# Kernel tuning notes

Hardware: AMD Instinct MI355X
Metric: run time of the kernel (lower is better)

Reference implementation:

```python
import jax, jax.numpy as jnp
import numpy as np

HEADS = 4
DIM_HEAD = 128


def setup_inputs() -> dict:
    key = jax.random.key(0)
    k1, k2, k3, k4 = jax.random.split(key, 4)
    b, dim, H, W = 4, 256, 128, 128
    hidden = HEADS * DIM_HEAD  # 512
    x = jax.random.normal(k1, (b, dim, H, W), dtype=jnp.float32)
    # 1x1 convs are pointwise matmuls over channels
    w_qkv = jax.random.normal(k2, (hidden * 3, dim), dtype=jnp.float32) * 0.02
    w_out = jax.random.normal(k3, (dim, hidden), dtype=jnp.float32) * 0.02
    b_out = jax.random.normal(k4, (dim,), dtype=jnp.float32) * 0.02
    return {"x": x, "w_qkv": w_qkv, "w_out": w_out, "b_out": b_out}


def reference(x, w_qkv, w_out, b_out):
    b, c, h, w = x.shape
    n = h * w
    # to_qkv: 1x1 conv (no bias) == channel matmul -> [b, 3*heads*dh, h, w]
    qkv = jnp.einsum('bchw,oc->bohw', x, w_qkv)
    # 'b (qkv heads d) h w -> qkv b heads d (h w)'
    qkv = qkv.reshape(b, 3, HEADS, DIM_HEAD, n)
    q, k, v = qkv[:, 0], qkv[:, 1], qkv[:, 2]  # each [b, heads, d, n]
    k = jax.nn.softmax(k, axis=-1)  # softmax over spatial positions
    context = jnp.einsum('bhdn,bhen->bhde', k, v)   # [b, heads, d, d]
    out = jnp.einsum('bhde,bhdn->bhen', context, q)  # [b, heads, d, n]
    out = out.reshape(b, HEADS * DIM_HEAD, h, w)
    # to_out: 1x1 conv with bias
    return jnp.einsum('bchw,oc->bohw', out, w_out) + b_out[None, :, None, None]
```

## Files before the change

### kernel.cpp

```cpp
#include <hip/hip_runtime.h>
#include <hip/hip_bf16.h>

#define HEADS 4
#define DH    128
#define CIN   256
#define NPIX  16384
#define NB    4
#define HID   512

typedef __attribute__((ext_vector_type(8))) short bf16x8;
typedef __attribute__((ext_vector_type(4))) float f32x4;

__device__ __forceinline__ unsigned short f2bfu(float f) {
    union { __hip_bfloat16 h; unsigned short u; } cv;
    cv.h = __float2bfloat16(f);
    return cv.u;
}

typedef const __attribute__((address_space(1))) unsigned char* gas_t;
typedef __attribute__((address_space(3))) unsigned char* las_t;
__device__ __forceinline__ void glds16(const void* g, void* s) {
    __builtin_amdgcn_global_load_lds((gas_t)g, (las_t)s, 16, 0, 0);
}


__global__ __launch_bounds__(256) void xt_convert2(const float* __restrict__ x,
                                                   unsigned short* __restrict__ xt2,
                                                   unsigned short* __restrict__ xbf2)
{
    __shared__ float tile[64][66];
    const int b = blockIdx.z, c0 = blockIdx.y * 64, n0 = blockIdx.x * 64;
    const int t = threadIdx.x, lane = t & 63, wid = t >> 6;
    const float* xb = x + ((size_t)b * CIN + c0) * NPIX + n0;
#pragma unroll
    for (int p = 0; p < 4; ++p) {
        const int c = p * 16 + (t >> 4);
        const int n = (t & 15) * 4;
        float4 v = *reinterpret_cast<const float4*>(xb + (size_t)c * NPIX + n);
        tile[c][n + 0] = v.x; tile[c][n + 1] = v.y;
        tile[c][n + 2] = v.z; tile[c][n + 3] = v.w;
    }
    __syncthreads();
#pragma unroll
    for (int rr = 0; rr < 2; ++rr) {
        const int tid  = wid * 2 + rr;
        const int n16l = tid >> 1, c32l = tid & 1;
        const int nl   = n16l * 16 + (lane & 15);
        const int cb   = c32l * 32 + (lane >> 4) * 8;
        unsigned short u8[8];
#pragma unroll
        for (int j = 0; j < 8; ++j) u8[j] = f2bfu(tile[cb + j][nl]);
        *reinterpret_cast<uint4*>(
            xt2 + (((size_t)b * 1024 + (n0 >> 4) + n16l) * 8 + (c0 >> 5) + c32l) * 512 + lane * 8)
            = *reinterpret_cast<const uint4*>(u8);
    }
#pragma unroll
    for (int rr = 0; rr < 2; ++rr) {
        const int tid  = wid * 2 + rr;
        const int c16l = tid >> 1, n32l = tid & 1;
        const int cr   = c16l * 16 + (lane & 15);
        const int nb   = n32l * 32 + (lane >> 4) * 8;
        unsigned short u8[8];
#pragma unroll
        for (int j = 0; j < 8; ++j) u8[j] = f2bfu(tile[cr][nb + j]);
        *reinterpret_cast<uint4*>(
            xbf2 + (((size_t)b * 16 + (c0 >> 4) + c16l) * 512 + (n0 >> 5) + n32l) * 512 + lane * 8)
            = *reinterpret_cast<const uint4*>(u8);
    }
}

__global__ __launch_bounds__(256) void wconv3(const float* __restrict__ w_qkv,
                                              const float* __restrict__ w_out,
                                              unsigned short* __restrict__ WkF,
                                              unsigned short* __restrict__ WvF,
                                              unsigned short* __restrict__ WqTF,
                                              unsigned short* __restrict__ WoF)
{
    const int t = threadIdx.x, lane = t & 63, wid = t >> 6;
    const int tile = blockIdx.x * 4 + wid;
    unsigned short u8[8];
    unsigned short* dst;
    if (tile < 256) {
        const int h = tile >> 6, d16 = (tile >> 3) & 7, c32 = tile & 7;
        const float* src = w_qkv + (size_t)(512 + h * 128 + d16 * 16 + (lane & 15)) * CIN
                         + c32 * 32 + (lane >> 4) * 8;
#pragma unroll
        for (int j = 0; j < 8; ++j) u8[j] = f2bfu(src[j]);
        dst = WkF + (size_t)tile * 512 + lane * 8;
    } else if (tile < 512) {
        const int t2 = tile - 256;
        const int h = t2 >> 6, e16 = (t2 >> 3) & 7, c32 = t2 & 7;
        const float* src = w_qkv + (size_t)(1024 + h * 128 + e16 * 16 + (lane & 15)) * CIN
                         + c32 * 32 + (lane >> 4) * 8;
#pragma unroll
        for (int j = 0; j < 8; ++j) u8[j] = f2bfu(src[j]);
        dst = WvF + (size_t)t2 * 512 + lane * 8;
    } else if (tile < 768) {
        const int t2 = tile - 512;
        const int h = t2 >> 6, c16 = (t2 >> 2) & 15, d32 = t2 & 3;
#pragma unroll
        for (int j = 0; j < 8; ++j)
            u8[j] = f2bfu(w_qkv[(size_t)(h * 128 + d32 * 32 + (lane >> 4) * 8 + j) * CIN
                                + c16 * 16 + (lane & 15)]);
        dst = WqTF + (size_t)t2 * 512 + lane * 8;
    } else {
        const int t2 = tile - 768;
        const int o16 = t2 >> 4, m32 = t2 & 15;
        const float* src = w_out + (size_t)(o16 * 16 + (lane & 15)) * HID
                         + m32 * 32 + (lane >> 4) * 8;
#pragma unroll
        for (int j = 0; j < 8; ++j) u8[j] = f2bfu(src[j]);
        dst = WoF + (size_t)t2 * 512 + lane * 8;
    }
    *reinterpret_cast<uint4*>(dst) = *reinterpret_cast<const uint4*>(u8);
}

__global__ __launch_bounds__(512, 2) void kg_fused6(const unsigned short* __restrict__ xt2,
                                                    const unsigned short* __restrict__ xbf2,
                                                    const unsigned short* __restrict__ WkF,
                                                    float* __restrict__ Gp,
                                                    float* __restrict__ S)
{
    __shared__ unsigned short sXT[2][32 * 512];
    __shared__ unsigned short sXB[2][32 * 512];
    __shared__ unsigned short sP[16 * 512];

    const int wgid = blockIdx.x;
    const int xcd  = wgid & 7;
    const int k_   = wgid >> 3;
    const int h    = k_ & 3;
    const int g_   = xcd + 8 * (k_ >> 2);
    const int ns   = g_ & 15;
    const int b    = g_ >> 4;
    const int bh   = b * 4 + h;

    const int t = threadIdx.x, lane = t & 63, wid = t >> 6;
    const int wm = wid >> 1, wn = wid & 1;
    const int wd = wid >> 2, wcq = wid & 3;
    const int cl = lane & 15, r0q = (lane >> 4) * 4;

    bf16x8 aW[2][8];
#pragma unroll
    for (int fi = 0; fi < 2; ++fi)
#pragma unroll
        for (int ks = 0; ks < 8; ++ks)
            aW[fi][ks] = *reinterpret_cast<const bf16x8*>(
                WkF + ((size_t)(h * 64 + (wm * 2 + fi) * 8 + ks)) * 512 + lane * 8);

    f32x4 accG[4][4] = {};
    float Sacc[8] = {};

    const unsigned short* xtb = xt2 + ((size_t)(b * 1024 + ns * 64) * 8) * 512;

#define STAGE_XT(nt_, buf_)                                                     \
    {                                                                           \
        const unsigned short* src_ = xtb + (size_t)(nt_) * 4 * 8 * 512;         \
        _Pragma("unroll")                                                       \
        for (int p = 0; p < 4; ++p) {                                           \
            const int tl = p * 8 + wid;                                         \
            glds16(src_ + (size_t)tl * 512 + lane * 8, sXT[buf_] + (size_t)tl * 512); \
        }                                                                       \
    }
#define STAGE_XB(nt_, buf_)                                                     \
    {                                                                           \
        const size_t nb32_ = (size_t)ns * 32 + (nt_) * 2;                       \
        _Pragma("unroll")                                                       \
        for (int p = 0; p < 4; ++p) {                                           \
            const int tl = p * 8 + wid;                                         \
            const int c16_ = tl >> 1, n32l_ = tl & 1;                           \
            glds16(xbf2 + (((size_t)(b * 16 + c16_)) * 512 + nb32_ + n32l_) * 512 + lane * 8, \
                   sXB[buf_] + (size_t)tl * 512);                               \
        }                                                                       \
    }

    STAGE_XT(0, 0);
    STAGE_XB(0, 0);
    __syncthreads();

    int cur = 0;
    for (int nt = 0; nt < 16; ++nt) {
        if (nt < 15) {
            STAGE_XT(nt + 1, cur ^ 1);
            STAGE_XB(nt + 1, cur ^ 1);
        }

        f32x4 acc1[2][2] = {};
#pragma unroll
        for (int ks = 0; ks < 8; ++ks) {
            bf16x8 bb[2];
#pragma unroll
            for (int fj = 0; fj < 2; ++fj)
                bb[fj] = *reinterpret_cast<const bf16x8*>(
                    &sXT[cur][((wn * 2 + fj) * 8 + ks) * 512 + lane * 8]);
#pragma unroll
            for (int fi = 0; fi < 2; ++fi)
#pragma unroll
                for (int fj = 0; fj < 2; ++fj)
                    acc1[fi][fj] = __builtin_amdgcn_mfma_f32_16x16x32_bf16(
                        aW[fi][ks], bb[fj], acc1[fi][fj], 0, 0, 0);
        }

#pragma unroll
        for (int fi = 0; fi < 2; ++fi)
#pragma unroll
            for (int r = 0; r < 4; ++r) {
                float rs = 0.f;
#pragma unroll
                for (int fj = 0; fj < 2; ++fj) {
                    const float v = __expf(acc1[fi][fj][r]);
                    rs += v;
                    const int us = ((r0q + r) + 16 * (fj * 2 + (cl >> 3))) * 8 + (cl & 7);
                    sP[((wm * 2 + fi) * 2 + wn) * 512 + us] = f2bfu(v);
                }
                Sacc[fi * 4 + r] += rs;
            }
        __syncthreads();

#pragma unroll
        for (int kn = 0; kn < 2; ++kn) {
            bf16x8 pa[4], bb[4];
#pragma unroll
            for (int fi = 0; fi < 4; ++fi)
                pa[fi] = *reinterpret_cast<const bf16x8*>(
                    &sP[((wd * 4 + fi) * 2 + kn) * 512 + lane * 8]);
#pragma unroll
            for (int fj = 0; fj < 4; ++fj)
                bb[fj] = *reinterpret_cast<const bf16x8*>(
                    &sXB[cur][((wcq * 4 + fj) * 2 + kn) * 512 + lane * 8]);
#pragma unroll
            for (int fi = 0; fi < 4; ++fi)
#pragma unroll
                for (int fj = 0; fj < 4; ++fj)
                    accG[fi][fj] = __builtin_amdgcn_mfma_f32_16x16x32_bf16(
                        pa[fi], bb[fj], accG[fi][fj], 0, 0, 0);
        }
        __syncthreads();
        cur ^= 1;
    }
#undef STAGE_XT
#undef STAGE_XB

#pragma unroll
    for (int i = 0; i < 8; ++i) {
        float v = Sacc[i];
        v += __shfl_xor(v, 1); v += __shfl_xor(v, 2);
        v += __shfl_xor(v, 4); v += __shfl_xor(v, 8);
        if (cl == 0) {
            const int d = wm * 32 + (i >> 2) * 16 + r0q + (i & 3);
            atomicAdd(&S[bh * 128 + d], v);
        }
    }

    float* gp = Gp + (size_t)(ns * 16 + bh) * (128 * 256);
#pragma unroll
    for (int fi = 0; fi < 4; ++fi)
#pragma unroll
        for (int fj = 0; fj < 4; ++fj)
#pragma unroll
            for (int r = 0; r < 4; ++r)
                gp[(size_t)(wd * 64 + fi * 16 + r0q + r) * 256 + wcq * 64 + fj * 16 + cl]
                    = accG[fi][fj][r];
}

__global__ __launch_bounds__(256) void g_reduce2(const float* __restrict__ Gp,
                                                 float* __restrict__ G)
{
    const int idx = blockIdx.x * 256 + threadIdx.x;
    const int bh = idx >> 15, dc = idx & 32767;
    float s = 0.f;
#pragma unroll
    for (int k = 0; k < 16; ++k)
        s += Gp[((size_t)k * 16 + bh) * 32768 + dc];
    G[idx] = s;
}

__global__ __launch_bounds__(256) void c1_kernel(const float* __restrict__ G,
                                                 const float* __restrict__ S,
                                                 const unsigned short* __restrict__ WvF,
                                                 const unsigned short* __restrict__ WqTF,
                                                 unsigned short* __restrict__ AbarF)
{
    __shared__ unsigned short sCtx[32 * 512];
    const int t = threadIdx.x, lane = t & 63, wid = t >> 6;
    const int bh = blockIdx.x, b = bh >> 2, h = bh & 3;
    const int cl = lane & 15, r0q = (lane >> 4) * 4;
    const int wr = wid >> 1, wc = wid & 1;
    const float* Gb = G + (size_t)bh * 32768;

    float invs[4];
#pragma unroll
    for (int fi = 0; fi < 4; ++fi)
        invs[fi] = 1.0f / S[bh * 128 + wr * 64 + fi * 16 + cl];

    f32x4 acc[4][4] = {};
#pragma unroll
    for (int ks = 0; ks < 8; ++ks) {
        bf16x8 a[4], bb[4];
#pragma unroll
        for (int fi = 0; fi < 4; ++fi) {
            const float* gp = Gb + (size_t)(wr * 64 + fi * 16 + cl) * 256
                            + ks * 32 + (lane >> 4) * 8;
            const float4 v0 = *reinterpret_cast<const float4*>(gp);
            const float4 v1 = *reinterpret_cast<const float4*>(gp + 4);
            unsigned short u8[8] = {
                f2bfu(v0.x * invs[fi]), f2bfu(v0.y * invs[fi]),
                f2bfu(v0.z * invs[fi]), f2bfu(v0.w * invs[fi]),
                f2bfu(v1.x * invs[fi]), f2bfu(v1.y * invs[fi]),
                f2bfu(v1.z * invs[fi]), f2bfu(v1.w * invs[fi]) };
            a[fi] = *reinterpret_cast<const bf16x8*>(u8);
        }
#pragma unroll
        for (int fj = 0; fj < 4; ++fj)
            bb[fj] = *reinterpret_cast<const bf16x8*>(
                WvF + ((size_t)(h * 8 + wc * 4 + fj) * 8 + ks) * 512 + lane * 8);
#pragma unroll
        for (int fi = 0; fi < 4; ++fi)
#pragma unroll
            for (int fj = 0; fj < 4; ++fj)
                acc[fi][fj] = __builtin_amdgcn_mfma_f32_16x16x32_bf16(
                    a[fi], bb[fj], acc[fi][fj], 0, 0, 0);
    }

#pragma unroll
    for (int fi = 0; fi < 4; ++fi)
#pragma unroll
        for (int fj = 0; fj < 4; ++fj)
#pragma unroll
            for (int r = 0; r < 4; ++r) {
                const int us = (cl + 16 * ((fi & 1) * 2 + ((r0q + r) >> 3))) * 8 + ((r0q + r) & 7);
                sCtx[((wc * 4 + fj) * 4 + wr * 2 + (fi >> 1)) * 512 + us] = f2bfu(acc[fi][fj][r]);
            }
    __syncthreads();

    const int we = wid >> 1, wcq = wid & 1;
    f32x4 acc2[4][8] = {};
#pragma unroll
    for (int ks = 0; ks < 4; ++ks) {
        bf16x8 a2[4], b2[8];
#pragma unroll
        for (int fi = 0; fi < 4; ++fi)
            a2[fi] = *reinterpret_cast<const bf16x8*>(
                &sCtx[((we * 4 + fi) * 4 + ks) * 512 + lane * 8]);
#pragma unroll
        for (int fj = 0; fj < 8; ++fj)
            b2[fj] = *reinterpret_cast<const bf16x8*>(
                WqTF + ((size_t)(h * 16 + wcq * 8 + fj) * 4 + ks) * 512 + lane * 8);
#pragma unroll
        for (int fi = 0; fi < 4; ++fi)
#pragma unroll
            for (int fj = 0; fj < 8; ++fj)
                acc2[fi][fj] = __builtin_amdgcn_mfma_f32_16x16x32_bf16(
                    a2[fi], b2[fj], acc2[fi][fj], 0, 0, 0);
    }

#pragma unroll
    for (int fi = 0; fi < 4; ++fi)
#pragma unroll
        for (int fj = 0; fj < 8; ++fj)
#pragma unroll
            for (int r = 0; r < 4; ++r) {
                const int c16 = wcq * 8 + fj;
                const int m32 = h * 4 + we * 2 + (fi >> 1);
                const int us  = (cl + 16 * ((fi & 1) * 2 + ((r0q + r) >> 3))) * 8 + ((r0q + r) & 7);
                AbarF[((size_t)(b * 16 + c16) * 16 + m32) * 512 + us] = f2bfu(acc2[fi][fj][r]);
            }
}

__global__ __launch_bounds__(256) void c2_kernel(const unsigned short* __restrict__ WoF,
                                                 const unsigned short* __restrict__ AbarF,
                                                 unsigned short* __restrict__ F2)
{
    const int t = threadIdx.x, lane = t & 63, wid = t >> 6;
    const int csp = blockIdx.x, b = blockIdx.y;
    const int cl = lane & 15, r0q = (lane >> 4) * 4;

    f32x4 acc[4][4] = {};
#pragma unroll
    for (int ks = 0; ks < 16; ++ks) {
        bf16x8 a[4], bb[4];
#pragma unroll
        for (int fi = 0; fi < 4; ++fi)
            a[fi] = *reinterpret_cast<const bf16x8*>(
                WoF + ((size_t)(wid * 4 + fi) * 16 + ks) * 512 + lane * 8);
#pragma unroll
        for (int fj = 0; fj < 4; ++fj)
            bb[fj] = *reinterpret_cast<const bf16x8*>(
                AbarF + ((size_t)(b * 16 + csp * 4 + fj) * 16 + ks) * 512 + lane * 8);
#pragma unroll
        for (int fi = 0; fi < 4; ++fi)
#pragma unroll
            for (int fj = 0; fj < 4; ++fj)
                acc[fi][fj] = __builtin_amdgcn_mfma_f32_16x16x32_bf16(
                    a[fi], bb[fj], acc[fi][fj], 0, 0, 0);
    }

#pragma unroll
    for (int fi = 0; fi < 4; ++fi)
#pragma unroll
        for (int fj = 0; fj < 4; ++fj)
#pragma unroll
            for (int r = 0; r < 4; ++r) {
                const int o16 = wid * 4 + fi;
                const int c32 = csp * 2 + (fj >> 1);
                const int us  = ((r0q + r) + 16 * ((fj & 1) * 2 + (cl >> 3))) * 8 + (cl & 7);
                F2[((size_t)(b * 16 + o16) * 8 + c32) * 512 + us] = f2bfu(acc[fi][fj][r]);
            }
}

__global__ __launch_bounds__(256, 2) void out_gemm3(const unsigned short* __restrict__ xt2,
                                                    const unsigned short* __restrict__ F2,
                                                    const float* __restrict__ b_out,
                                                    float* __restrict__ out)
{
    __shared__ unsigned short sXT[64 * 512];
    const int t = threadIdx.x, lane = t & 63, wid = t >> 6;
    const int n0 = blockIdx.x * 128, m0 = blockIdx.y * 128, b = blockIdx.z;
    const int wr = wid >> 1, wc = wid & 1;

    const unsigned short* src = xt2 + ((size_t)(b * 1024 + (n0 >> 4)) * 8) * 512;
#pragma unroll
    for (int p = 0; p < 16; ++p) {
        const int tl = p * 4 + wid;
        glds16(src + (size_t)tl * 512 + lane * 8, sXT + (size_t)tl * 512);
    }
    __syncthreads();

    f32x4 acc[4][4] = {};
#pragma unroll
    for (int ks = 0; ks < 8; ++ks) {
        bf16x8 a[4], bb[4];
#pragma unroll
        for (int fi = 0; fi < 4; ++fi)
            a[fi] = *reinterpret_cast<const bf16x8*>(
                F2 + (((size_t)b * 16 + (m0 >> 4) + wr * 4 + fi) * 8 + ks) * 512 + lane * 8);
#pragma unroll
        for (int fj = 0; fj < 4; ++fj)
            bb[fj] = *reinterpret_cast<const bf16x8*>(
                &sXT[((wc * 4 + fj) * 8 + ks) * 512 + lane * 8]);
#pragma unroll
        for (int fi = 0; fi < 4; ++fi)
#pragma unroll
            for (int fj = 0; fj < 4; ++fj)
                acc[fi][fj] = __builtin_amdgcn_mfma_f32_16x16x32_bf16(
                    a[fi], bb[fj], acc[fi][fj], 0, 0, 0);
    }

    const int col = lane & 15, r0q = (lane >> 4) * 4;
#pragma unroll
    for (int fi = 0; fi < 4; ++fi)
#pragma unroll
        for (int r = 0; r < 4; ++r) {
            const int o = m0 + wr * 64 + fi * 16 + r0q + r;
            const float bias = b_out[o];
#pragma unroll
            for (int fj = 0; fj < 4; ++fj)
                out[((size_t)b * CIN + o) * NPIX + n0 + wc * 64 + fj * 16 + col] =
                    acc[fi][fj][r] + bias;
        }
}

extern "C" void kernel_launch(void* const* d_in, const int* in_sizes, int n_in,
                              void* d_out, int out_size, void* d_ws, size_t ws_size,
                              hipStream_t stream)
{
    const float* x     = (const float*)d_in[0];
    const float* w_qkv = (const float*)d_in[1];
    const float* w_out = (const float*)d_in[2];
    const float* b_out = (const float*)d_in[3];
    float* out = (float*)d_out;

    char* ws = (char*)d_ws;
    unsigned short* xt2   = (unsigned short*)ws;
    unsigned short* xbf2  = (unsigned short*)(ws + (32ull << 20));
    unsigned short* WkF   = (unsigned short*)(ws + (64ull << 20));
    unsigned short* WvF   = (unsigned short*)(ws + (64ull << 20) + (256u << 10));
    unsigned short* WqTF  = (unsigned short*)(ws + (64ull << 20) + (512u << 10));
    unsigned short* WoF   = (unsigned short*)(ws + (64ull << 20) + (768u << 10));
    float*          S     = (float*)(ws + (65ull << 20));
    float*          G     = (float*)(ws + (66ull << 20));
    unsigned short* AbarF = (unsigned short*)(ws + (68ull << 20));
    unsigned short* F2    = (unsigned short*)(ws + (69ull << 20));
    float*          Gp    = (float*)(ws + (72ull << 20));

    hipMemsetAsync(S, 0, 2048 * sizeof(float), stream);
    xt_convert2<<<dim3(NPIX / 64, CIN / 64, NB), 256, 0, stream>>>(x, xt2, xbf2);
    wconv3<<<256, 256, 0, stream>>>(w_qkv, w_out, WkF, WvF, WqTF, WoF);
    kg_fused6<<<256, 512, 0, stream>>>(xt2, xbf2, WkF, Gp, S);
    g_reduce2<<<2048, 256, 0, stream>>>(Gp, G);
    c1_kernel<<<16, 256, 0, stream>>>(G, S, WvF, WqTF, AbarF);
    c2_kernel<<<dim3(4, NB), 256, 0, stream>>>(WoF, AbarF, F2);
    out_gemm3<<<dim3(NPIX / 128, CIN / 128, NB), 256, 0, stream>>>(xt2, F2, b_out, out);
}
```

Measured before the change: 136.0 us.

## Store one bf16 copy of x and read transposed fragments with ds_read_tr

The conversion kernel now writes a single bf16 packed layout of x instead of two transposed copies. The fused K/G kernel stages one buffer and builds the transposed B operand with ds_read_b64_tr_b16 LDS transpose reads, and the output GEMM reads the new layout as well. This halves the bf16 intermediate write and read traffic and the LDS staging footprint. The launch bound hint rises to 4 blocks per CU. The risk is LDS bank conflicts or serialization from the explicit waitcnt and sched_barrier around the transpose reads.

```diff
diff --git a/kernel.cpp b/kernel.cpp
--- a/kernel.cpp
+++ b/kernel.cpp
@@ -10,6 +10,7 @@
 
 typedef __attribute__((ext_vector_type(8))) short bf16x8;
 typedef __attribute__((ext_vector_type(4))) float f32x4;
+typedef __attribute__((ext_vector_type(2))) unsigned u32x2;
 
 __device__ __forceinline__ unsigned short f2bfu(float f) {
     union { __hip_bfloat16 h; unsigned short u; } cv;
@@ -22,15 +23,17 @@
 __device__ __forceinline__ void glds16(const void* g, void* s) {
     __builtin_amdgcn_global_load_lds((gas_t)g, (las_t)s, 16, 0, 0);
 }
-
-
-__global__ __launch_bounds__(256) void xt_convert2(const float* __restrict__ x,
-                                                   unsigned short* __restrict__ xt2,
-                                                   unsigned short* __restrict__ xbf2)
-{
-    __shared__ float tile[64][66];
+__device__ __forceinline__ unsigned lds_off(const void* p) {
+    return (unsigned)(size_t)(las_t)p;
+}
+
+
+__global__ __launch_bounds__(256) void xp_convert(const float* __restrict__ x,
+                                                  unsigned short* __restrict__ xp)
+{
+    __shared__ float tile[64][67];
     const int b = blockIdx.z, c0 = blockIdx.y * 64, n0 = blockIdx.x * 64;
-    const int t = threadIdx.x, lane = t & 63, wid = t >> 6;
+    const int t = threadIdx.x;
     const float* xb = x + ((size_t)b * CIN + c0) * NPIX + n0;
 #pragma unroll
     for (int p = 0; p < 4; ++p) {
@@ -41,32 +44,15 @@
         tile[c][n + 2] = v.z; tile[c][n + 3] = v.w;
     }
     __syncthreads();
-#pragma unroll
-    for (int rr = 0; rr < 2; ++rr) {
-        const int tid  = wid * 2 + rr;
-        const int n16l = tid >> 1, c32l = tid & 1;
-        const int nl   = n16l * 16 + (lane & 15);
-        const int cb   = c32l * 32 + (lane >> 4) * 8;
-        unsigned short u8[8];
-#pragma unroll
-        for (int j = 0; j < 8; ++j) u8[j] = f2bfu(tile[cb + j][nl]);
-        *reinterpret_cast<uint4*>(
-            xt2 + (((size_t)b * 1024 + (n0 >> 4) + n16l) * 8 + (c0 >> 5) + c32l) * 512 + lane * 8)
-            = *reinterpret_cast<const uint4*>(u8);
-    }
-#pragma unroll
-    for (int rr = 0; rr < 2; ++rr) {
-        const int tid  = wid * 2 + rr;
-        const int c16l = tid >> 1, n32l = tid & 1;
-        const int cr   = c16l * 16 + (lane & 15);
-        const int nb   = n32l * 32 + (lane >> 4) * 8;
-        unsigned short u8[8];
-#pragma unroll
-        for (int j = 0; j < 8; ++j) u8[j] = f2bfu(tile[cr][nb + j]);
-        *reinterpret_cast<uint4*>(
-            xbf2 + (((size_t)b * 16 + (c0 >> 4) + c16l) * 512 + (n0 >> 5) + n32l) * 512 + lane * 8)
-            = *reinterpret_cast<const uint4*>(u8);
-    }
+    const int n16l = t >> 6, c16l = (t >> 4) & 3, n_loc = t & 15;
+    unsigned short u16[16];
+#pragma unroll
+    for (int j = 0; j < 16; ++j)
+        u16[j] = f2bfu(tile[c16l * 16 + j][n16l * 16 + n_loc]);
+    unsigned short* dst = xp + (((size_t)(b * 1024 + (n0 >> 4) + n16l)) * 16
+                                + (c0 >> 4) + c16l) * 256 + n_loc * 16;
+    *reinterpret_cast<uint4*>(dst)     = *reinterpret_cast<const uint4*>(u16);
+    *reinterpret_cast<uint4*>(dst + 8) = *reinterpret_cast<const uint4*>(u16 + 8);
 }
 
 __global__ __launch_bounds__(256) void wconv3(const float* __restrict__ w_qkv,
@@ -115,14 +101,12 @@
     *reinterpret_cast<uint4*>(dst) = *reinterpret_cast<const uint4*>(u8);
 }
 
-__global__ __launch_bounds__(512, 2) void kg_fused6(const unsigned short* __restrict__ xt2,
-                                                    const unsigned short* __restrict__ xbf2,
+__global__ __launch_bounds__(512, 4) void kg_fused7(const unsigned short* __restrict__ xp,
                                                     const unsigned short* __restrict__ WkF,
                                                     float* __restrict__ Gp,
                                                     float* __restrict__ S)
 {
-    __shared__ unsigned short sXT[2][32 * 512];
-    __shared__ unsigned short sXB[2][32 * 512];
+    __shared__ unsigned short sX[2][64 * 256];
     __shared__ unsigned short sP[16 * 512];
 
     const int wgid = blockIdx.x;
@@ -137,7 +121,9 @@
     const int t = threadIdx.x, lane = t & 63, wid = t >> 6;
     const int wm = wid >> 1, wn = wid & 1;
     const int wd = wid >> 2, wcq = wid & 3;
-    const int cl = lane & 15, r0q = (lane >> 4) * 4;
+    const int cl = lane & 15, q = lane >> 4, r0q = q * 4;
+    const int boff  = cl * 16 + (q & 1) * 8 + (q >> 1) * 256;
+    const unsigned troff = (unsigned)((q >> 1) * 8192 + (q & 1) * 256 + cl * 8);
 
     bf16x8 aW[2][8];
 #pragma unroll
@@ -150,39 +136,23 @@
     f32x4 accG[4][4] = {};
     float Sacc[8] = {};
 
-    const unsigned short* xtb = xt2 + ((size_t)(b * 1024 + ns * 64) * 8) * 512;
-
-#define STAGE_XT(nt_, buf_)                                                     \
+    const unsigned short* xpb = xp + ((size_t)(b * 1024 + ns * 64) * 16) * 256;
+
+#define STAGE(nt_, buf_)                                                        \
     {                                                                           \
-        const unsigned short* src_ = xtb + (size_t)(nt_) * 4 * 8 * 512;         \
+        const unsigned short* src_ = xpb + (size_t)(nt_) * 16384;               \
         _Pragma("unroll")                                                       \
-        for (int p = 0; p < 4; ++p) {                                           \
-            const int tl = p * 8 + wid;                                         \
-            glds16(src_ + (size_t)tl * 512 + lane * 8, sXT[buf_] + (size_t)tl * 512); \
-        }                                                                       \
-    }
-#define STAGE_XB(nt_, buf_)                                                     \
-    {                                                                           \
-        const size_t nb32_ = (size_t)ns * 32 + (nt_) * 2;                       \
-        _Pragma("unroll")                                                       \
-        for (int p = 0; p < 4; ++p) {                                           \
-            const int tl = p * 8 + wid;                                         \
-            const int c16_ = tl >> 1, n32l_ = tl & 1;                           \
-            glds16(xbf2 + (((size_t)(b * 16 + c16_)) * 512 + nb32_ + n32l_) * 512 + lane * 8, \
-                   sXB[buf_] + (size_t)tl * 512);                               \
-        }                                                                       \
-    }
-
-    STAGE_XT(0, 0);
-    STAGE_XB(0, 0);
+        for (int p = 0; p < 4; ++p)                                             \
+            glds16(src_ + ((size_t)p * 512 + t) * 8,                            \
+                   &sX[buf_][((size_t)p * 512 + wid * 64) * 8]);                \
+    }
+
+    STAGE(0, 0);
     __syncthreads();
 
     int cur = 0;
     for (int nt = 0; nt < 16; ++nt) {
-        if (nt < 15) {
-            STAGE_XT(nt + 1, cur ^ 1);
-            STAGE_XB(nt + 1, cur ^ 1);
-        }
+        if (nt < 15) STAGE(nt + 1, cur ^ 1);
 
         f32x4 acc1[2][2] = {};
 #pragma unroll
@@ -191,7 +161,7 @@
 #pragma unroll
             for (int fj = 0; fj < 2; ++fj)
                 bb[fj] = *reinterpret_cast<const bf16x8*>(
-                    &sXT[cur][((wn * 2 + fj) * 8 + ks) * 512 + lane * 8]);
+                    &sX[cur][((wn * 2 + fj) * 16 + 2 * ks) * 256 + boff]);
 #pragma unroll
             for (int fi = 0; fi < 2; ++fi)
 #pragma unroll
@@ -216,29 +186,44 @@
             }
         __syncthreads();
 
-#pragma unroll
-        for (int kn = 0; kn < 2; ++kn) {
-            bf16x8 pa[4], bb[4];
-#pragma unroll
-            for (int fi = 0; fi < 4; ++fi)
-                pa[fi] = *reinterpret_cast<const bf16x8*>(
-                    &sP[((wd * 4 + fi) * 2 + kn) * 512 + lane * 8]);
-#pragma unroll
-            for (int fj = 0; fj < 4; ++fj)
-                bb[fj] = *reinterpret_cast<const bf16x8*>(
-                    &sXB[cur][((wcq * 4 + fj) * 2 + kn) * 512 + lane * 8]);
-#pragma unroll
-            for (int fi = 0; fi < 4; ++fi)
-#pragma unroll
-                for (int fj = 0; fj < 4; ++fj)
-                    accG[fi][fj] = __builtin_amdgcn_mfma_f32_16x16x32_bf16(
-                        pa[fi], bb[fj], accG[fi][fj], 0, 0, 0);
+        {
+            const unsigned sx_base = lds_off(&sX[cur][0]);
+#pragma unroll
+            for (int kn = 0; kn < 2; ++kn) {
+                u32x2 lo[4], hi[4];
+#pragma unroll
+                for (int fj = 0; fj < 4; ++fj) {
+                    const int cc = wcq * 4 + fj;
+                    const unsigned a = sx_base + (unsigned)((kn * 32 + cc) * 512) + troff;
+                    asm volatile("ds_read_b64_tr_b16 %0, %2\n\t"
+                                 "ds_read_b64_tr_b16 %1, %2 offset:128"
+                                 : "=&v"(lo[fj]), "=&v"(hi[fj])
+                                 : "v"(a));
+                }
+                asm volatile("s_waitcnt lgkmcnt(0)" ::: "memory");
+                __builtin_amdgcn_sched_barrier(0);
+
+                bf16x8 pa[4];
+#pragma unroll
+                for (int fi = 0; fi < 4; ++fi)
+                    pa[fi] = *reinterpret_cast<const bf16x8*>(
+                        &sP[((wd * 4 + fi) * 2 + kn) * 512 + lane * 8]);
+#pragma unroll
+                for (int fj = 0; fj < 4; ++fj) {
+                    union { bf16x8 v; u32x2 h2[2]; } fb;
+                    fb.h2[0] = lo[fj];
+                    fb.h2[1] = hi[fj];
+#pragma unroll
+                    for (int fi = 0; fi < 4; ++fi)
+                        accG[fi][fj] = __builtin_amdgcn_mfma_f32_16x16x32_bf16(
+                            pa[fi], fb.v, accG[fi][fj], 0, 0, 0);
+                }
+            }
         }
         __syncthreads();
         cur ^= 1;
     }
-#undef STAGE_XT
-#undef STAGE_XB
+#undef STAGE
 
 #pragma unroll
     for (int i = 0; i < 8; ++i) {
@@ -407,22 +392,22 @@
             }
 }
 
-__global__ __launch_bounds__(256, 2) void out_gemm3(const unsigned short* __restrict__ xt2,
+__global__ __launch_bounds__(256, 2) void out_gemm4(const unsigned short* __restrict__ xp,
                                                     const unsigned short* __restrict__ F2,
                                                     const float* __restrict__ b_out,
                                                     float* __restrict__ out)
 {
-    __shared__ unsigned short sXT[64 * 512];
+    __shared__ unsigned short sXT[128 * 256];
     const int t = threadIdx.x, lane = t & 63, wid = t >> 6;
     const int n0 = blockIdx.x * 128, m0 = blockIdx.y * 128, b = blockIdx.z;
     const int wr = wid >> 1, wc = wid & 1;
-
-    const unsigned short* src = xt2 + ((size_t)(b * 1024 + (n0 >> 4)) * 8) * 512;
-#pragma unroll
-    for (int p = 0; p < 16; ++p) {
-        const int tl = p * 4 + wid;
-        glds16(src + (size_t)tl * 512 + lane * 8, sXT + (size_t)tl * 512);
-    }
+    const int cl = lane & 15, q = lane >> 4;
+    const int boff = cl * 16 + (q & 1) * 8 + (q >> 1) * 256;
+
+    const unsigned short* src = xp + ((size_t)(b * 1024 + (n0 >> 4)) * 16) * 256;
+#pragma unroll
+    for (int p = 0; p < 16; ++p)
+        glds16(src + ((size_t)p * 256 + t) * 8, &sXT[((size_t)p * 256 + wid * 64) * 8]);
     __syncthreads();
 
     f32x4 acc[4][4] = {};
@@ -436,7 +421,7 @@
 #pragma unroll
         for (int fj = 0; fj < 4; ++fj)
             bb[fj] = *reinterpret_cast<const bf16x8*>(
-                &sXT[((wc * 4 + fj) * 8 + ks) * 512 + lane * 8]);
+                &sXT[((wc * 4 + fj) * 16 + 2 * ks) * 256 + boff]);
 #pragma unroll
         for (int fi = 0; fi < 4; ++fi)
 #pragma unroll
@@ -445,7 +430,7 @@
                     a[fi], bb[fj], acc[fi][fj], 0, 0, 0);
     }
 
-    const int col = lane & 15, r0q = (lane >> 4) * 4;
+    const int r0q = q * 4;
 #pragma unroll
     for (int fi = 0; fi < 4; ++fi)
 #pragma unroll
@@ -454,7 +439,7 @@
             const float bias = b_out[o];
 #pragma unroll
             for (int fj = 0; fj < 4; ++fj)
-                out[((size_t)b * CIN + o) * NPIX + n0 + wc * 64 + fj * 16 + col] =
+                out[((size_t)b * CIN + o) * NPIX + n0 + wc * 64 + fj * 16 + cl] =
                     acc[fi][fj][r] + bias;
         }
 }
@@ -470,8 +455,7 @@
     float* out = (float*)d_out;
 
     char* ws = (char*)d_ws;
-    unsigned short* xt2   = (unsigned short*)ws;
-    unsigned short* xbf2  = (unsigned short*)(ws + (32ull << 20));
+    unsigned short* xp    = (unsigned short*)ws;
     unsigned short* WkF   = (unsigned short*)(ws + (64ull << 20));
     unsigned short* WvF   = (unsigned short*)(ws + (64ull << 20) + (256u << 10));
     unsigned short* WqTF  = (unsigned short*)(ws + (64ull << 20) + (512u << 10));
@@ -483,11 +467,11 @@
     float*          Gp    = (float*)(ws + (72ull << 20));
 
     hipMemsetAsync(S, 0, 2048 * sizeof(float), stream);
-    xt_convert2<<<dim3(NPIX / 64, CIN / 64, NB), 256, 0, stream>>>(x, xt2, xbf2);
+    xp_convert<<<dim3(NPIX / 64, CIN / 64, NB), 256, 0, stream>>>(x, xp);
     wconv3<<<256, 256, 0, stream>>>(w_qkv, w_out, WkF, WvF, WqTF, WoF);
-    kg_fused6<<<256, 512, 0, stream>>>(xt2, xbf2, WkF, Gp, S);
+    kg_fused7<<<256, 512, 0, stream>>>(xp, WkF, Gp, S);
     g_reduce2<<<2048, 256, 0, stream>>>(Gp, G);
     c1_kernel<<<16, 256, 0, stream>>>(G, S, WvF, WqTF, AbarF);
     c2_kernel<<<dim3(4, NB), 256, 0, stream>>>(WoF, AbarF, F2);
-    out_gemm3<<<dim3(NPIX / 128, CIN / 128, NB), 256, 0, stream>>>(xt2, F2, b_out, out);
-}
+    out_gemm4<<<dim3(NPIX / 128, CIN / 128, NB), 256, 0, stream>>>(xp, F2, b_out, out);
+}
```

New measurement: 203.8 us. +49.8%, slower.
